# Kernel tuning notes

Measured on AMD Instinct MI355X. Metric: run time of the kernel, lower is better.

The kernel has to match this reference:

```python
import jax, jax.numpy as jnp
import numpy as np

MAX_DEPTH = 8
LMBDA = 0.1
OUTPUT_DIM = 128


def setup_inputs() -> dict:
    key = jax.random.key(0)
    k1, k2, k3, k4, k5, k6 = jax.random.split(key, 6)
    B, D, C = 8192, 2048, OUTPUT_DIM
    n_inner = 2 ** MAX_DEPTH - 1  # 255 inner nodes, BFS order
    n_leaf = 2 ** MAX_DEPTH       # 256 leaves
    x = jax.random.normal(k1, (B, D), dtype=jnp.float32)
    target = jax.random.randint(k2, (B,), 0, C)
    # small scale so sigmoid gates are not saturated (log(pen), log(1-pen) finite)
    W = jax.random.normal(k3, (n_inner, D), dtype=jnp.float32) * 0.02
    b = jax.random.normal(k4, (n_inner,), dtype=jnp.float32) * 0.02
    beta = jax.random.normal(k5, (n_inner,), dtype=jnp.float32)
    leaf_params = jax.random.normal(k6, (n_leaf, C), dtype=jnp.float32)
    return {"x": x, "target": target, "W": W, "b": b, "beta": beta,
            "leaf_params": leaf_params}


def reference(x, target, W, b, beta, leaf_params):
    B = x.shape[0]
    C = leaf_params.shape[1]
    y = jax.nn.one_hot(target, C, dtype=x.dtype)  # target_onehot

    # All inner-node gates as one batched GEMM: p[b,i] = sigmoid(beta_i*(x@w_i+b_i))
    p = jax.nn.sigmoid(beta[None, :] * (x @ W.T + b[None, :]))  # [B, n_inner]

    # Level-by-level path probability propagation (BFS node order).
    path = jnp.ones((B, 1), x.dtype)
    penalties = []  # per-level [2^d] node penalties
    start = 0
    for d in range(MAX_DEPTH):
        n = 2 ** d
        p_lvl = p[:, start:start + n]                      # [B, 2^d]
        pen = jnp.sum(p_lvl * path, axis=0) / jnp.sum(path, axis=0)
        penalties.append(pen)
        # left child gets path*(1-p), right gets path*p; interleave -> next level
        path = jnp.stack([path * (1.0 - p_lvl), path * p_lvl], axis=-1).reshape(B, 2 * n)
        start += n
    # path: [B, n_leaf] leaf path probabilities (left-to-right order)

    Q = jax.nn.softmax(leaf_params, axis=-1)               # [n_leaf, C]
    TQ = y @ jnp.log(Q).T                                  # [B, n_leaf], y . log Q per leaf
    loss = jnp.mean(jnp.sum(path * TQ, axis=1))

    # Penalty C: only inner nodes whose children are NOT leaves contribute
    # (original get_penalty drops depth==max_depth nodes), depths 1..max_depth-1.
    Cpen = jnp.asarray(0.0, x.dtype)
    for d in range(MAX_DEPTH - 1):
        lam = LMBDA * 2.0 ** (-(d + 1))
        pen = penalties[d]
        Cpen = Cpen - lam * 0.5 * jnp.sum(jnp.log(pen) + jnp.log(1.0 - pen))

    total = -loss + Cpen

    # output: Q of the max-path-prob leaf per sample
    leaf_idx = jnp.argmax(path, axis=1)                    # [B]
    output = Q[leaf_idx]                                   # [B, C]
    return total, output
```

## Files before the change

kernel.cpp:

```cpp
#include <hip/hip_runtime.h>
#include <hip/hip_bf16.h>
#include <hip/hip_fp16.h>
#include <stdint.h>

#define B_SIZE 8192
#define D_SIZE 2048
#define C_SIZE 128
#define N_INNER 255
#define N_LEAF 256
#define NPAD 256
#define NBLK_PATH 512

typedef _Float16 half8 __attribute__((ext_vector_type(8)));
typedef __fp16 pk16x2 __attribute__((ext_vector_type(2)));
typedef float f32x4 __attribute__((ext_vector_type(4)));
typedef unsigned short u16;

__device__ inline uint32_t pkh(float a, float b) {
    pk16x2 h = __builtin_amdgcn_cvt_pkrtz(a, b);
    return __builtin_bit_cast(uint32_t, h);
}
__device__ inline void split4(const float4 v, uint2& hi, uint2& lo) {
    pk16x2 a01 = __builtin_amdgcn_cvt_pkrtz(v.x, v.y);
    pk16x2 a23 = __builtin_amdgcn_cvt_pkrtz(v.z, v.w);
    float r0 = v.x - (float)a01[0];
    float r1 = v.y - (float)a01[1];
    float r2 = v.z - (float)a23[0];
    float r3 = v.w - (float)a23[1];
    hi = make_uint2(__builtin_bit_cast(uint32_t, a01), __builtin_bit_cast(uint32_t, a23));
    lo = make_uint2(pkh(r0, r1), pkh(r2, r3));
}
__device__ inline void splitB8(const float4 v0, const float4 v1, half8& h, half8& l) {
    uint2 h0, l0, h1, l1;
    split4(v0, h0, l0);
    split4(v1, h1, l1);
    uint4 hh = make_uint4(h0.x, h0.y, h1.x, h1.y);
    uint4 ll = make_uint4(l0.x, l0.y, l1.x, l1.y);
    h = __builtin_bit_cast(half8, hh);
    l = __builtin_bit_cast(half8, ll);
}

__global__ __launch_bounds__(256) void prep_kernel(
    const float* __restrict__ lp, float* __restrict__ Q, float* __restrict__ logQt)
{
    int row = blockIdx.x;
    int t = threadIdx.x;
    __shared__ float red[128];
    float v = 0.f;
    if (t < 128) { v = lp[row * C_SIZE + t]; red[t] = v; }
    __syncthreads();
    for (int s = 64; s > 0; s >>= 1) { if (t < s) red[t] = fmaxf(red[t], red[t + s]); __syncthreads(); }
    float mx = red[0]; __syncthreads();
    float e = 0.f;
    if (t < 128) { e = expf(v - mx); red[t] = e; }
    __syncthreads();
    for (int s = 64; s > 0; s >>= 1) { if (t < s) red[t] += red[t + s]; __syncthreads(); }
    float sum = red[0];
    if (t < 128) {
        Q[row * C_SIZE + t] = e / sum;
        logQt[(size_t)t * N_LEAF + row] = (v - mx) - logf(sum);
    }
}

#define GBM 64
#define GBK 32
#define GKSPLIT 4
#define KCHUNK (D_SIZE / GKSPLIT)
#define KITERS (KCHUNK / GBK)
#define LDKA 40

__global__ __launch_bounds__(256, 2) void gemm_mfma(
    const float* __restrict__ x, const float* __restrict__ W,
    float* __restrict__ zp)
{
    __shared__ __align__(16) u16 sAh[4][GBM * LDKA];
    __shared__ __align__(16) u16 sAl[4][GBM * LDKA];

    const int t = threadIdx.x;
    const int lane = t & 63, w = t >> 6;
    const int lr = lane & 15, lq = lane >> 4;
    const int mi = blockIdx.x >> 2;
    const int kz = blockIdx.x & 3;
    const int m0 = mi * GBM;
    const int kb0 = kz * KCHUNK;

    f32x4 acc[4][4];
    #pragma unroll
    for (int mt = 0; mt < 4; ++mt)
        #pragma unroll
        for (int nt = 0; nt < 4; ++nt) acc[mt][nt] = (f32x4){0.f, 0.f, 0.f, 0.f};

    int brow[4];
    #pragma unroll
    for (int nt = 0; nt < 4; ++nt) {
        int rrow = w * 64 + nt * 16 + lr;
        brow[nt] = (rrow > 254) ? 254 : rrow;
    }

    float4 av_c[8];
    #pragma unroll
    for (int i = 0; i < 8; ++i) {
        int idx = i * 64 + lane;
        int row = idx >> 3, ch = idx & 7;
        av_c[i] = *(const float4*)(x + (size_t)(m0 + row) * D_SIZE + kb0 + ch * 4);
    }
    half8 bh[4], bl[4];
    #pragma unroll
    for (int nt = 0; nt < 4; ++nt) {
        const float* p = W + (size_t)brow[nt] * D_SIZE + kb0 + lq * 8;
        float4 b0 = *(const float4*)(p);
        float4 b1 = *(const float4*)(p + 4);
        splitB8(b0, b1, bh[nt], bl[nt]);
    }

    #pragma unroll
    for (int kt = 0; kt < KITERS; ++kt) {
        const int kb = kb0 + kt * GBK;
        float4 nb0[4], nb1[4];
        if (kt + 1 < KITERS) {
            #pragma unroll
            for (int nt = 0; nt < 4; ++nt) {
                const float* p = W + (size_t)brow[nt] * D_SIZE + kb + GBK + lq * 8;
                nb0[nt] = *(const float4*)(p);
                nb1[nt] = *(const float4*)(p + 4);
            }
        }
        float4 av_n[8];
        if (kt + 1 < KITERS) {
            #pragma unroll
            for (int i = 0; i < 8; ++i) {
                int idx = i * 64 + lane;
                int row = idx >> 3, ch = idx & 7;
                av_n[i] = *(const float4*)(x + (size_t)(m0 + row) * D_SIZE + kb + GBK + ch * 4);
            }
        }
        #pragma unroll
        for (int i = 0; i < 8; ++i) {
            int idx = i * 64 + lane;
            int row = idx >> 3, ch = idx & 7;
            uint2 hi, lo; split4(av_c[i], hi, lo);
            *(uint2*)&sAh[w][row * LDKA + ch * 4] = hi;
            *(uint2*)&sAl[w][row * LDKA + ch * 4] = lo;
        }
        asm volatile("s_waitcnt lgkmcnt(0)" ::: "memory");
        half8 ah[4], al[4];
        #pragma unroll
        for (int mt = 0; mt < 4; ++mt) {
            int off = (mt * 16 + lr) * LDKA + lq * 8;
            ah[mt] = *(const half8*)&sAh[w][off];
            al[mt] = *(const half8*)&sAl[w][off];
        }
        #pragma unroll
        for (int mt = 0; mt < 4; ++mt)
            #pragma unroll
            for (int nt = 0; nt < 4; ++nt) {
                acc[mt][nt] = __builtin_amdgcn_mfma_f32_16x16x32_f16(ah[mt], bh[nt], acc[mt][nt], 0, 0, 0);
                acc[mt][nt] = __builtin_amdgcn_mfma_f32_16x16x32_f16(ah[mt], bl[nt], acc[mt][nt], 0, 0, 0);
                acc[mt][nt] = __builtin_amdgcn_mfma_f32_16x16x32_f16(al[mt], bh[nt], acc[mt][nt], 0, 0, 0);
            }
        if (kt + 1 < KITERS) {
            #pragma unroll
            for (int i = 0; i < 8; ++i) av_c[i] = av_n[i];
            #pragma unroll
            for (int nt = 0; nt < 4; ++nt) splitB8(nb0[nt], nb1[nt], bh[nt], bl[nt]);
        }
    }

    float* zout = zp + (size_t)kz * B_SIZE * NPAD;
    #pragma unroll
    for (int mt = 0; mt < 4; ++mt) {
        #pragma unroll
        for (int nt = 0; nt < 4; ++nt) {
            int gn = w * 64 + nt * 16 + lr;
            #pragma unroll
            for (int r = 0; r < 4; ++r) {
                int gm = m0 + mt * 16 + lq * 4 + r;
                zout[(size_t)gm * NPAD + gn] = acc[mt][nt][r];
            }
        }
    }
}

__global__ __launch_bounds__(256) void path_kernel(
    const float* __restrict__ z, const int* __restrict__ target,
    const float* __restrict__ bvec, const float* __restrict__ beta,
    const float* __restrict__ Q, const float* __restrict__ logQt,
    float* __restrict__ partial, float* __restrict__ out)
{
    __shared__ float pbuf[4][256];
    __shared__ float s_num[128], s_den[128], s_loss;
    const int t = threadIdx.x, w = t >> 6, lane = t & 63;
    const int c0 = lane * 4;
    float pnum[4] = {0.f, 0.f, 0.f, 0.f};
    float pden[4] = {0.f, 0.f, 0.f, 0.f};
    float loss = 0.f;

    if (t < 128) s_num[t] = 0.f;
    else s_den[t - 128] = 0.f;
    if (t == 0) s_loss = 0.f;
    __syncthreads();

    float bet[4], bia[4];
    #pragma unroll
    for (int j = 0; j < 4; ++j) {
        int c = c0 + j;
        bet[j] = (c < N_INNER) ? beta[c] : 0.f;
        bia[j] = (c < N_INNER) ? bvec[c] : 0.f;
    }

    for (int i = 0; i < 4; ++i) {
        int r = blockIdx.x * 16 + w * 4 + i;
        float4 s = make_float4(0.f, 0.f, 0.f, 0.f);
        #pragma unroll
        for (int p = 0; p < GKSPLIT; ++p) {
            float4 v = *(const float4*)(z + ((size_t)p * B_SIZE + r) * NPAD + c0);
            s.x += v.x; s.y += v.y; s.z += v.z; s.w += v.w;
        }
        float zv[4] = {s.x, s.y, s.z, s.w};
        float pv[4];
        #pragma unroll
        for (int j = 0; j < 4; ++j) {
            int c = c0 + j;
            pv[j] = (c < N_INNER) ? 1.f / (1.f + expf(-bet[j] * (zv[j] + bia[j]))) : 0.f;
        }
        *(float4*)&pbuf[w][c0] = make_float4(pv[0], pv[1], pv[2], pv[3]);
        asm volatile("s_waitcnt lgkmcnt(0)" ::: "memory");

        int tg = target[r];
        float4 lq4 = *(const float4*)(logQt + (size_t)tg * N_LEAF + c0);
        float lqa[4] = {lq4.x, lq4.y, lq4.z, lq4.w};

        float P = 1.f;
        #pragma unroll
        for (int d = 0; d < 6; ++d) {
            int node = (1 << d) - 1 + (c0 >> (8 - d));
            int bit = (c0 >> (7 - d)) & 1;
            float pvn = pbuf[w][node];
            P *= bit ? pvn : (1.f - pvn);
        }
        float p6  = pbuf[w][63 + lane];
        float p7a = pbuf[w][127 + 2 * lane];
        float p7b = pbuf[w][127 + 2 * lane + 1];
        float lsum = 0.f, bestV = -1.f;
        int bestI = 0;
        #pragma unroll
        for (int j = 0; j < 4; ++j) {
            float t6 = (j & 2) ? p6 : (1.f - p6);
            float p7 = (j & 2) ? p7b : p7a;
            float t7 = (j & 1) ? p7 : (1.f - p7);
            float pl = (P * t6) * t7;
            lsum += pl * lqa[j];
            if (pl > bestV) { bestV = pl; bestI = c0 + j; }
        }
        if (lane < 32) {
            #pragma unroll
            for (int j = 0; j < 4; ++j) {
                int c = c0 + j;
                if (c < 127) {
                    int h = c + 1; int d = 31 - __clz(h);
                    float pp = 1.f;
                    for (int e = 0; e < d; ++e) {
                        int ha = h >> (d - e);
                        int bit = (h >> (d - 1 - e)) & 1;
                        float pvn = pbuf[w][ha - 1];
                        pp *= bit ? pvn : (1.f - pvn);
                    }
                    pnum[j] += pbuf[w][c] * pp;
                    pden[j] += pp;
                }
            }
        }
        #pragma unroll
        for (int m = 1; m < 64; m <<= 1) {
            lsum += __shfl_xor(lsum, m, 64);
            float ov = __shfl_xor(bestV, m, 64);
            int   oi = __shfl_xor(bestI, m, 64);
            if (ov > bestV || (ov == bestV && oi < bestI)) { bestV = ov; bestI = oi; }
        }
        loss += lsum;
        out[1 + (size_t)r * C_SIZE + lane]      = Q[bestI * C_SIZE + lane];
        out[1 + (size_t)r * C_SIZE + lane + 64] = Q[bestI * C_SIZE + lane + 64];
        asm volatile("" ::: "memory");
    }

    if (lane < 32) {
        #pragma unroll
        for (int j = 0; j < 4; ++j) {
            int c = c0 + j;
            if (c < 127) {
                atomicAdd(&s_num[c], pnum[j]);
                atomicAdd(&s_den[c], pden[j]);
            }
        }
    }
    if (lane == 0) atomicAdd(&s_loss, loss);
    __syncthreads();
    float* rec = partial + (size_t)blockIdx.x * 256;
    if (t < 127)        rec[t] = s_num[t];
    else if (t == 127)  rec[127] = s_loss;
    else if (t < 255)   rec[t] = s_den[t - 128];
    else                rec[255] = 0.f;
}

__global__ __launch_bounds__(1024) void reduce_kernel(
    const float* __restrict__ partial, float* __restrict__ out)
{
    __shared__ float part[4][256];
    __shared__ float s[256];
    __shared__ float red[128];
    const int t = threadIdx.x;
    const int col = t & 255, seg = t >> 8;
    const int base = seg * (NBLK_PATH / 4);
    float a0 = 0.f, a1 = 0.f, a2 = 0.f, a3 = 0.f;
    for (int r = 0; r < NBLK_PATH / 4; r += 4) {
        a0 += partial[(size_t)(base + r + 0) * 256 + col];
        a1 += partial[(size_t)(base + r + 1) * 256 + col];
        a2 += partial[(size_t)(base + r + 2) * 256 + col];
        a3 += partial[(size_t)(base + r + 3) * 256 + col];
    }
    part[seg][col] = (a0 + a1) + (a2 + a3);
    __syncthreads();
    if (t < 256) s[t] = (part[0][t] + part[1][t]) + (part[2][t] + part[3][t]);
    __syncthreads();
    float term = 0.f;
    if (t < 127) {
        int d = 31 - __clz(t + 1);
        float lam = 0.1f * exp2f(-(float)(d + 1));
        float pen = s[t] / s[128 + t];
        term = lam * 0.5f * (logf(pen) + logf(1.f - pen));
    }
    if (t < 128) { red[t] = term; }
    __syncthreads();
    for (int sh = 64; sh > 0; sh >>= 1) { if (t < sh) red[t] += red[t + sh]; __syncthreads(); }
    if (t == 0) out[0] = -(s[127] / (float)B_SIZE) - red[0];
}

extern "C" void kernel_launch(void* const* d_in, const int* in_sizes, int n_in,
                              void* d_out, int out_size, void* d_ws, size_t ws_size,
                              hipStream_t stream)
{
    const float* x    = (const float*)d_in[0];
    const int*   tgt  = (const int*)d_in[1];
    const float* W    = (const float*)d_in[2];
    const float* b    = (const float*)d_in[3];
    const float* beta = (const float*)d_in[4];
    const float* lp   = (const float*)d_in[5];
    float* out = (float*)d_out;

    float* z       = (float*)d_ws;
    float* Q       = z + (size_t)GKSPLIT * B_SIZE * NPAD;
    float* logQt   = Q + (size_t)N_LEAF * C_SIZE;
    float* partial = logQt + (size_t)C_SIZE * N_LEAF;

    prep_kernel<<<256, 256, 0, stream>>>(lp, Q, logQt);

    gemm_mfma<<<512, 256, 0, stream>>>(x, W, z);

    path_kernel<<<NBLK_PATH, 256, 0, stream>>>(
        z, tgt, b, beta, Q, logQt, partial, out);

    reduce_kernel<<<1, 1024, 0, stream>>>(partial, out);
}
```

Before: 168.1 us.

## Fuse softmax prep into GEMM launch and batch path-kernel loads per warp

Removes the separate prep kernel by having 256 extra blocks of the GEMM launch compute the leaf softmax and log-softmax, saving one launch. Separately, the path kernel now issues all four rows' z-partial loads, target loads and logQt gathers up front, using a larger shared pbuf so each row has its own slot and the loads can overlap instead of serializing per row. The cost is more shared memory and registers per block in the path kernel, plus the GEMM kernel reserving shared memory for prep blocks.

```diff
diff --git a/kernel.cpp b/kernel.cpp
--- a/kernel.cpp
+++ b/kernel.cpp
@@ -40,28 +40,6 @@
     l = __builtin_bit_cast(half8, ll);
 }
 
-__global__ __launch_bounds__(256) void prep_kernel(
-    const float* __restrict__ lp, float* __restrict__ Q, float* __restrict__ logQt)
-{
-    int row = blockIdx.x;
-    int t = threadIdx.x;
-    __shared__ float red[128];
-    float v = 0.f;
-    if (t < 128) { v = lp[row * C_SIZE + t]; red[t] = v; }
-    __syncthreads();
-    for (int s = 64; s > 0; s >>= 1) { if (t < s) red[t] = fmaxf(red[t], red[t + s]); __syncthreads(); }
-    float mx = red[0]; __syncthreads();
-    float e = 0.f;
-    if (t < 128) { e = expf(v - mx); red[t] = e; }
-    __syncthreads();
-    for (int s = 64; s > 0; s >>= 1) { if (t < s) red[t] += red[t + s]; __syncthreads(); }
-    float sum = red[0];
-    if (t < 128) {
-        Q[row * C_SIZE + t] = e / sum;
-        logQt[(size_t)t * N_LEAF + row] = (v - mx) - logf(sum);
-    }
-}
-
 #define GBM 64
 #define GBK 32
 #define GKSPLIT 4
@@ -69,14 +47,35 @@
 #define KITERS (KCHUNK / GBK)
 #define LDKA 40
 
-__global__ __launch_bounds__(256, 2) void gemm_mfma(
-    const float* __restrict__ x, const float* __restrict__ W,
-    float* __restrict__ zp)
+__global__ __launch_bounds__(256, 2) void gemm_prep(
+    const float* __restrict__ x, const float* __restrict__ W, float* __restrict__ zp,
+    const float* __restrict__ lp, float* __restrict__ Q, float* __restrict__ logQt)
 {
     __shared__ __align__(16) u16 sAh[4][GBM * LDKA];
     __shared__ __align__(16) u16 sAl[4][GBM * LDKA];
+    __shared__ float red[128];
 
     const int t = threadIdx.x;
+
+    if (blockIdx.x >= 512) {
+        int row = blockIdx.x - 512;
+        float v = 0.f;
+        if (t < 128) { v = lp[row * C_SIZE + t]; red[t] = v; }
+        __syncthreads();
+        for (int s = 64; s > 0; s >>= 1) { if (t < s) red[t] = fmaxf(red[t], red[t + s]); __syncthreads(); }
+        float mx = red[0]; __syncthreads();
+        float e = 0.f;
+        if (t < 128) { e = expf(v - mx); red[t] = e; }
+        __syncthreads();
+        for (int s = 64; s > 0; s >>= 1) { if (t < s) red[t] += red[t + s]; __syncthreads(); }
+        float sum = red[0];
+        if (t < 128) {
+            Q[row * C_SIZE + t] = e / sum;
+            logQt[(size_t)t * N_LEAF + row] = (v - mx) - logf(sum);
+        }
+        return;
+    }
+
     const int lane = t & 63, w = t >> 6;
     const int lr = lane & 15, lq = lane >> 4;
     const int mi = blockIdx.x >> 2;
@@ -187,7 +186,7 @@
     const float* __restrict__ Q, const float* __restrict__ logQt,
     float* __restrict__ partial, float* __restrict__ out)
 {
-    __shared__ float pbuf[4][256];
+    __shared__ float pbuf[16][256];
     __shared__ float s_num[128], s_den[128], s_loss;
     const int t = threadIdx.x, w = t >> 6, lane = t & 63;
     const int c0 = lane * 4;
@@ -208,39 +207,57 @@
         bia[j] = (c < N_INNER) ? bvec[c] : 0.f;
     }
 
+    const int rbase = blockIdx.x * 16 + w * 4;
+
+    float4 zs[4];
+    #pragma unroll
     for (int i = 0; i < 4; ++i) {
-        int r = blockIdx.x * 16 + w * 4 + i;
         float4 s = make_float4(0.f, 0.f, 0.f, 0.f);
         #pragma unroll
         for (int p = 0; p < GKSPLIT; ++p) {
-            float4 v = *(const float4*)(z + ((size_t)p * B_SIZE + r) * NPAD + c0);
+            float4 v = *(const float4*)(z + ((size_t)p * B_SIZE + rbase + i) * NPAD + c0);
             s.x += v.x; s.y += v.y; s.z += v.z; s.w += v.w;
         }
-        float zv[4] = {s.x, s.y, s.z, s.w};
+        zs[i] = s;
+    }
+    int tg[4];
+    #pragma unroll
+    for (int i = 0; i < 4; ++i) tg[i] = target[rbase + i];
+
+    #pragma unroll
+    for (int i = 0; i < 4; ++i) {
+        float zv[4] = {zs[i].x, zs[i].y, zs[i].z, zs[i].w};
         float pv[4];
         #pragma unroll
         for (int j = 0; j < 4; ++j) {
             int c = c0 + j;
             pv[j] = (c < N_INNER) ? 1.f / (1.f + expf(-bet[j] * (zv[j] + bia[j]))) : 0.f;
         }
-        *(float4*)&pbuf[w][c0] = make_float4(pv[0], pv[1], pv[2], pv[3]);
-        asm volatile("s_waitcnt lgkmcnt(0)" ::: "memory");
-
-        int tg = target[r];
-        float4 lq4 = *(const float4*)(logQt + (size_t)tg * N_LEAF + c0);
-        float lqa[4] = {lq4.x, lq4.y, lq4.z, lq4.w};
+        *(float4*)&pbuf[w * 4 + i][c0] = make_float4(pv[0], pv[1], pv[2], pv[3]);
+    }
+    float4 lq[4];
+    #pragma unroll
+    for (int i = 0; i < 4; ++i)
+        lq[i] = *(const float4*)(logQt + (size_t)tg[i] * N_LEAF + c0);
+    asm volatile("s_waitcnt lgkmcnt(0)" ::: "memory");
+
+    #pragma unroll
+    for (int i = 0; i < 4; ++i) {
+        const float* pb = pbuf[w * 4 + i];
+        const int r = rbase + i;
+        float lqa[4] = {lq[i].x, lq[i].y, lq[i].z, lq[i].w};
 
         float P = 1.f;
         #pragma unroll
         for (int d = 0; d < 6; ++d) {
             int node = (1 << d) - 1 + (c0 >> (8 - d));
             int bit = (c0 >> (7 - d)) & 1;
-            float pvn = pbuf[w][node];
+            float pvn = pb[node];
             P *= bit ? pvn : (1.f - pvn);
         }
-        float p6  = pbuf[w][63 + lane];
-        float p7a = pbuf[w][127 + 2 * lane];
-        float p7b = pbuf[w][127 + 2 * lane + 1];
+        float p6  = pb[63 + lane];
+        float p7a = pb[127 + 2 * lane];
+        float p7b = pb[127 + 2 * lane + 1];
         float lsum = 0.f, bestV = -1.f;
         int bestI = 0;
         #pragma unroll
@@ -262,10 +279,10 @@
                     for (int e = 0; e < d; ++e) {
                         int ha = h >> (d - e);
                         int bit = (h >> (d - 1 - e)) & 1;
-                        float pvn = pbuf[w][ha - 1];
+                        float pvn = pb[ha - 1];
                         pp *= bit ? pvn : (1.f - pvn);
                     }
-                    pnum[j] += pbuf[w][c] * pp;
+                    pnum[j] += pb[c] * pp;
                     pden[j] += pp;
                 }
             }
@@ -280,7 +297,6 @@
         loss += lsum;
         out[1 + (size_t)r * C_SIZE + lane]      = Q[bestI * C_SIZE + lane];
         out[1 + (size_t)r * C_SIZE + lane + 64] = Q[bestI * C_SIZE + lane + 64];
-        asm volatile("" ::: "memory");
     }
 
     if (lane < 32) {
@@ -352,9 +368,7 @@
     float* logQt   = Q + (size_t)N_LEAF * C_SIZE;
     float* partial = logQt + (size_t)C_SIZE * N_LEAF;
 
-    prep_kernel<<<256, 256, 0, stream>>>(lp, Q, logQt);
-
-    gemm_mfma<<<512, 256, 0, stream>>>(x, W, z);
+    gemm_prep<<<768, 256, 0, stream>>>(x, W, z, lp, Q, logQt);
 
     path_kernel<<<NBLK_PATH, 256, 0, stream>>>(
         z, tgt, b, beta, Q, logQt, partial, out);
```

Measured after the change: 166.7 us. About the same (-0.9%).
